# Kernel optimization log

Measured on AMD Instinct MI355X. Metric: run time of the kernel, lower is better.

The kernel has to match this reference:

```python
import jax, jax.numpy as jnp
import numpy as np

N = 100000
IN_F = 165
HID = 128
E = 1600000


def gcn_conv(x, W, b, src, dst, n):
    # PyG GCNConv: h = x @ W; add self-loops; symmetric norm D^-1/2 A D^-1/2; aggregate; + bias
    h = x @ W  # [n, out]
    src_sl = jnp.concatenate([src, jnp.arange(n)])
    dst_sl = jnp.concatenate([dst, jnp.arange(n)])
    deg = jax.ops.segment_sum(jnp.ones_like(src_sl, dtype=h.dtype), dst_sl, num_segments=n)
    dinv = jnp.where(deg > 0, jax.lax.rsqrt(deg), 0.0)
    norm = dinv[src_sl] * dinv[dst_sl]  # [e+n]
    msg = h[src_sl] * norm[:, None]
    out = jax.ops.segment_sum(msg, dst_sl, num_segments=n)
    return out + b


def setup_inputs() -> dict:
    key = jax.random.key(0)
    k = jax.random.split(key, 8)
    x = jax.random.normal(k[0], (N, IN_F), dtype=jnp.float32)
    edge_index = jax.random.randint(k[1], (2, E), 0, N)
    s1 = 1.0 / np.sqrt(IN_F)
    s2 = 1.0 / np.sqrt(HID)
    W1 = jax.random.uniform(k[2], (IN_F, HID), jnp.float32, -s1, s1)
    b1 = jnp.zeros((HID,), jnp.float32)
    W2 = jax.random.uniform(k[3], (HID, HID), jnp.float32, -s2, s2)
    b2 = jnp.zeros((HID,), jnp.float32)
    Wc = jax.random.uniform(k[4], (HID, 2), jnp.float32, -s2, s2)
    bc = jax.random.uniform(k[5], (2,), jnp.float32, -s2, s2)
    return {"x": x, "edge_index": edge_index, "W1": W1, "b1": b1,
            "W2": W2, "b2": b2, "Wc": Wc, "bc": bc}


def reference(x, edge_index, W1, b1, W2, b2, Wc, bc):
    src, dst = edge_index[0], edge_index[1]
    h = jax.nn.relu(gcn_conv(x, W1, b1, src, dst, N))
    # dropout inactive (eval mode)
    h = jax.nn.relu(gcn_conv(h, W2, b2, src, dst, N))
    return h @ Wc + bc
```

## Files before the change

### kernel.cpp

```cpp
#include <hip/hip_runtime.h>


typedef _Float16 half8 __attribute__((ext_vector_type(8)));
typedef float floatx4 __attribute__((ext_vector_type(4)));
typedef float f4u __attribute__((ext_vector_type(4), aligned(4)));

#define SLOT_C 64
#define BCAP 4608
#define NBKT 391
#define CHUNK 4096

__global__ __launch_bounds__(256) void multisplit_k(const int* __restrict__ src,
                                                    const int* __restrict__ dst, int e,
                                                    int* __restrict__ bcnt,
                                                    int2* __restrict__ edges2) {
  __shared__ int lhist[NBKT];
  __shared__ int lbase[NBKT];
  __shared__ int lcur[NBKT];
  int t = threadIdx.x;
  int e0 = blockIdx.x * CHUNK;
  int e1 = min(e0 + CHUNK, e);
  for (int b = t; b < NBKT; b += 256) { lhist[b] = 0; lcur[b] = 0; }
  __syncthreads();
  for (int i = e0 + t; i < e1; i += 256)
    atomicAdd(&lhist[dst[i] >> 8], 1);
  __syncthreads();
  for (int b = t; b < NBKT; b += 256) {
    int h = lhist[b];
    lbase[b] = h ? atomicAdd(&bcnt[b], h) : 0;
  }
  __syncthreads();
  for (int i = e0 + t; i < e1; i += 256) {
    int d = dst[i];
    int b = d >> 8;
    int p = lbase[b] + atomicAdd(&lcur[b], 1);
    if (p < BCAP) edges2[(size_t)b * BCAP + p] = make_int2(src[i], d);
  }
}

__global__ __launch_bounds__(256) void csr_from_bins_k(const int2* __restrict__ edges2,
                                                       const int* __restrict__ bcnt,
                                                       int* __restrict__ cnt_g,
                                                       int* __restrict__ csr,
                                                       float* __restrict__ dinv, int n) {
  __shared__ int lcnt[256];
  int b = blockIdx.x;
  int node0 = b << 8;
  int t = threadIdx.x;
  lcnt[t] = 0;
  __syncthreads();
  int ec = min(bcnt[b], BCAP);
  const int2* ebase = edges2 + (size_t)b * BCAP;
  for (int i = t; i < ec; i += 256) {
    int2 ed = ebase[i];
    int p = atomicAdd(&lcnt[ed.y - node0], 1);
    if (p < SLOT_C) csr[((size_t)ed.y << 6) + p] = ed.x;
  }
  __syncthreads();
  int node = node0 + t;
  if (node < n) {
    int c = lcnt[t];
    cnt_g[node] = c;
    dinv[node] = rsqrtf((float)(c + 1));
  }
}

__global__ void w_split_k(const float* __restrict__ W, int K, int Kpad,
                          _Float16* __restrict__ WhT, _Float16* __restrict__ WlT) {
  int idx = blockIdx.x * blockDim.x + threadIdx.x;
  if (idx >= 128 * Kpad) return;
  int c = idx / Kpad, k = idx - c * Kpad;
  float v = (k < K) ? W[(size_t)k * 128 + c] : 0.f;
  _Float16 h = (_Float16)v;
  WhT[idx] = h;
  WlT[idx] = (_Float16)(v - (float)h);
}

template <bool AHALF>
__global__ __launch_bounds__(256) void gemm_f16_k(const void* __restrict__ Av,
                                                  const _Float16* __restrict__ WhT,
                                                  const _Float16* __restrict__ WlT,
                                                  const float* __restrict__ rowscale,
                                                  _Float16* __restrict__ out,
                                                  int n, int K, int Kpad) {
  int wave = threadIdx.x >> 6, lane = threadIdx.x & 63;
  int m = lane & 15, quad = lane >> 4;
  int rowblk = blockIdx.x >> 1;
  int cbase = (blockIdx.x & 1) * 4;
  int rowbase = rowblk * 64 + wave * 16;
  int ra = min(rowbase + m, n - 1);

  floatx4 acc[4];
#pragma unroll
  for (int c = 0; c < 4; ++c) acc[c] = (floatx4){0.f, 0.f, 0.f, 0.f};

  const int nslab = Kpad >> 5;

  f4u xa0, xa1, xb0, xb1;
  half8 ha, hb;

  auto loadA = [&](int s, f4u& x0, f4u& x1, half8& h) {
    int k0 = (s << 5) + quad * 8;
    if constexpr (AHALF) {
      const _Float16* arow = (const _Float16*)Av + (size_t)ra * K;
      h = *(const half8*)(arow + k0);
    } else {
      const float* arow = (const float*)Av + (size_t)ra * K;
      if ((s << 5) + 32 <= K) {
        x0 = *(const f4u*)(arow + k0);
        x1 = *(const f4u*)(arow + k0 + 4);
      } else {
#pragma unroll
        for (int j = 0; j < 4; ++j) { int kk = k0 + j;     kk = kk < K ? kk : K - 1; x0[j] = arow[kk]; }
#pragma unroll
        for (int j = 0; j < 4; ++j) { int kk = k0 + 4 + j; kk = kk < K ? kk : K - 1; x1[j] = arow[kk]; }
      }
    }
  };

  auto loadW = [&](int s, half8 (&wh)[4], half8 (&wl)[4]) {
    int k0 = (s << 5) + quad * 8;
#pragma unroll
    for (int c = 0; c < 4; ++c) {
      size_t o = (size_t)((cbase + c) * 16 + m) * Kpad + k0;
      wh[c] = *(const half8*)(WhT + o);
      wl[c] = *(const half8*)(WlT + o);
    }
  };

  auto doSlab = [&](const half8 (&wh)[4], const half8 (&wl)[4],
                    const f4u& x0, const f4u& x1, const half8& h) {
    half8 ah, al;
    if constexpr (AHALF) {
      ah = h;
    } else {
#pragma unroll
      for (int j = 0; j < 8; ++j) {
        float v = (j < 4) ? x0[j] : x1[j - 4];
        _Float16 hh = (_Float16)v;
        ah[j] = hh;
        al[j] = (_Float16)(v - (float)hh);
      }
    }
#pragma unroll
    for (int c = 0; c < 4; ++c) {
      acc[c] = __builtin_amdgcn_mfma_f32_16x16x32_f16(ah, wh[c], acc[c], 0, 0, 0);
      acc[c] = __builtin_amdgcn_mfma_f32_16x16x32_f16(ah, wl[c], acc[c], 0, 0, 0);
      if constexpr (!AHALF)
        acc[c] = __builtin_amdgcn_mfma_f32_16x16x32_f16(al, wh[c], acc[c], 0, 0, 0);
    }
  };

  loadA(0, xa0, xa1, ha);
  for (int s = 0; s < nslab; s += 2) {
    half8 wh0[4], wl0[4];
    loadW(s, wh0, wl0);
    loadA(s + 1, xb0, xb1, hb);
    doSlab(wh0, wl0, xa0, xa1, ha);
    half8 wh1[4], wl1[4];
    loadW(s + 1, wh1, wl1);
    if (s + 2 < nslab) loadA(s + 2, xa0, xa1, ha);
    doSlab(wh1, wl1, xb0, xb1, hb);
  }

#pragma unroll
  for (int i = 0; i < 4; ++i) {
    int row = rowbase + quad * 4 + i;
    if (row < n) {
      float di = rowscale ? rowscale[row] : 1.0f;
#pragma unroll
      for (int c = 0; c < 4; ++c)
        out[(size_t)row * 128 + (cbase + c) * 16 + m] = (_Float16)(acc[c][i] * di);
    }
  }
}

template <bool CLS>
__global__ __launch_bounds__(256) void aggregate_k(const _Float16* __restrict__ g,
                                                   const int* __restrict__ cnt,
                                                   const int* __restrict__ csr,
                                                   const float* __restrict__ dinv,
                                                   const float* __restrict__ bias,
                                                   const float* __restrict__ Wc,
                                                   const float* __restrict__ bc,
                                                   _Float16* __restrict__ out16,
                                                   float* __restrict__ out32, int n) {
  int wave = threadIdx.x >> 6;
  int lane = threadIdx.x & 63;
  int i = blockIdx.x * 4 + wave;
  if (i >= n) return;
  int qtr = lane >> 4;
  int l16 = lane & 15;
  int f = l16 * 8;

  float acc[8];
#pragma unroll
  for (int j = 0; j < 8; ++j) acc[j] = 0.f;

  int deg = min(cnt[i], SLOT_C);
  size_t s0 = (size_t)i << 6;

  if (deg > 0) {
    int last = deg - 1;
    for (int eb = 0; eb < deg; eb += 16) {
#pragma unroll
      for (int k = 0; k < 4; ++k) {
        int ee = eb + 4 * k + qtr;
        float w = (ee <= last) ? 1.f : 0.f;
        int ec = (ee <= last) ? ee : last;
        int srow = csr[s0 + ec];
        half8 v = *(const half8*)&g[(size_t)srow * 128 + f];
#pragma unroll
        for (int j = 0; j < 8; ++j) acc[j] = fmaf(w, (float)v[j], acc[j]);
      }
    }
#pragma unroll
    for (int j = 0; j < 8; ++j) {
      acc[j] += __shfl_xor(acc[j], 16, 64);
      acc[j] += __shfl_xor(acc[j], 32, 64);
    }
  }

  half8 self = *(const half8*)&g[(size_t)i * 128 + f];
  float di = dinv[i];
  float4 b0 = *(const float4*)&bias[f];
  float4 b1 = *(const float4*)&bias[f + 4];
  float bv[8] = {b0.x, b0.y, b0.z, b0.w, b1.x, b1.y, b1.z, b1.w};
  float r[8];
#pragma unroll
  for (int j = 0; j < 8; ++j)
    r[j] = fmaxf((acc[j] + (float)self[j]) * di + bv[j], 0.f);

  if (!CLS) {
    if (qtr == 0) {
      half8 o;
#pragma unroll
      for (int j = 0; j < 8; ++j) o[j] = (_Float16)(r[j] * di);
      *(half8*)&out16[(size_t)i * 128 + f] = o;
    }
  } else {
    float c0v = 0.f, c1v = 0.f;
#pragma unroll
    for (int q = 0; q < 4; ++q) {
      float4 wv = *(const float4*)&Wc[f * 2 + q * 4];
      c0v += r[q * 2] * wv.x + r[q * 2 + 1] * wv.z;
      c1v += r[q * 2] * wv.y + r[q * 2 + 1] * wv.w;
    }
#pragma unroll
    for (int off = 8; off > 0; off >>= 1) {
      c0v += __shfl_down(c0v, off, 16);
      c1v += __shfl_down(c1v, off, 16);
    }
    if (lane == 0) {
      out32[(size_t)i * 2 + 0] = c0v + bc[0];
      out32[(size_t)i * 2 + 1] = c1v + bc[1];
    }
  }
}

extern "C" void kernel_launch(void* const* d_in, const int* in_sizes, int n_in,
                              void* d_out, int out_size, void* d_ws, size_t ws_size,
                              hipStream_t stream) {
  const float* x  = (const float*)d_in[0];
  const int*   ei = (const int*)d_in[1];
  const float* W1 = (const float*)d_in[2];
  const float* b1 = (const float*)d_in[3];
  const float* W2 = (const float*)d_in[4];
  const float* b2 = (const float*)d_in[5];
  const float* Wc = (const float*)d_in[6];
  const float* bc = (const float*)d_in[7];
  float* out = (float*)d_out;

  const int IN_F = 165;
  const int KP1 = 192;
  const int n = in_sizes[0] / IN_F;
  const int e = in_sizes[1] / 2;
  const int* src = ei;
  const int* dst = ei + e;

  char* ws = (char*)d_ws;
  size_t off = 0;
  auto alloc = [&](size_t bytes) -> void* {
    void* p = ws + off;
    off += (bytes + 255) & ~(size_t)255;
    return p;
  };
  _Float16* bufA = (_Float16*)alloc((size_t)n * 128 * 2);
  _Float16* bufB = (_Float16*)alloc((size_t)n * 128 * 2);
  int*   csr  = (int*)alloc((size_t)n * SLOT_C * 4);
  int2*  edges2 = (int2*)alloc((size_t)NBKT * BCAP * 8);
  int*   cnt  = (int*)alloc((size_t)n * 4);
  int*   bcnt = (int*)alloc((size_t)NBKT * 4);
  float* dinv = (float*)alloc((size_t)n * 4);
  _Float16* w1h = (_Float16*)alloc((size_t)128 * KP1 * 2);
  _Float16* w1l = (_Float16*)alloc((size_t)128 * KP1 * 2);
  _Float16* w2h = (_Float16*)alloc((size_t)128 * 128 * 2);
  _Float16* w2l = (_Float16*)alloc((size_t)128 * 128 * 2);

  hipMemsetAsync(bcnt, 0, (size_t)NBKT * 4, stream);

  const int tb = 256;
  w_split_k<<<(128 * KP1 + tb - 1) / tb, tb, 0, stream>>>(W1, IN_F, KP1, w1h, w1l);
  w_split_k<<<(128 * 128 + tb - 1) / tb, tb, 0, stream>>>(W2, 128, 128, w2h, w2l);

  multisplit_k<<<(e + CHUNK - 1) / CHUNK, 256, 0, stream>>>(src, dst, e, bcnt, edges2);
  csr_from_bins_k<<<NBKT, 256, 0, stream>>>(edges2, bcnt, cnt, csr, dinv, n);

  const int gemmgrid = 2 * ((n + 63) / 64);
  gemm_f16_k<false><<<gemmgrid, 256, 0, stream>>>(x, w1h, w1l, dinv, bufA, n, IN_F, KP1);
  aggregate_k<false><<<(n + 3) / 4, 256, 0, stream>>>(bufA, cnt, csr, dinv, b1, nullptr, nullptr,
                                                      bufB, nullptr, n);
  gemm_f16_k<true><<<gemmgrid, 256, 0, stream>>>(bufB, w2h, w2l, nullptr, bufA, n, 128, 128);
  aggregate_k<true><<<(n + 3) / 4, 256, 0, stream>>>(bufA, cnt, csr, dinv, b2, Wc, bc,
                                                     nullptr, out, n);
}
```

Measured before the change: 415.3 us.

## Compute all 128 output columns per GEMM block to reuse A loads

```diff
diff --git a/kernel.cpp b/kernel.cpp
--- a/kernel.cpp
+++ b/kernel.cpp
@@ -77,22 +77,20 @@
 }
 
 template <bool AHALF>
-__global__ __launch_bounds__(256) void gemm_f16_k(const void* __restrict__ Av,
-                                                  const _Float16* __restrict__ WhT,
-                                                  const _Float16* __restrict__ WlT,
-                                                  const float* __restrict__ rowscale,
-                                                  _Float16* __restrict__ out,
-                                                  int n, int K, int Kpad) {
+__global__ __launch_bounds__(256, 4) void gemm_f16_k(const void* __restrict__ Av,
+                                                     const _Float16* __restrict__ WhT,
+                                                     const _Float16* __restrict__ WlT,
+                                                     const float* __restrict__ rowscale,
+                                                     _Float16* __restrict__ out,
+                                                     int n, int K, int Kpad) {
   int wave = threadIdx.x >> 6, lane = threadIdx.x & 63;
   int m = lane & 15, quad = lane >> 4;
-  int rowblk = blockIdx.x >> 1;
-  int cbase = (blockIdx.x & 1) * 4;
-  int rowbase = rowblk * 64 + wave * 16;
+  int rowbase = blockIdx.x * 64 + wave * 16;
   int ra = min(rowbase + m, n - 1);
 
-  floatx4 acc[4];
-#pragma unroll
-  for (int c = 0; c < 4; ++c) acc[c] = (floatx4){0.f, 0.f, 0.f, 0.f};
+  floatx4 acc[8];
+#pragma unroll
+  for (int c = 0; c < 8; ++c) acc[c] = (floatx4){0.f, 0.f, 0.f, 0.f};
 
   const int nslab = Kpad >> 5;
 
@@ -118,49 +116,55 @@
     }
   };
 
-  auto loadW = [&](int s, half8 (&wh)[4], half8 (&wl)[4]) {
-    int k0 = (s << 5) + quad * 8;
-#pragma unroll
-    for (int c = 0; c < 4; ++c) {
-      size_t o = (size_t)((cbase + c) * 16 + m) * Kpad + k0;
-      wh[c] = *(const half8*)(WhT + o);
-      wl[c] = *(const half8*)(WlT + o);
-    }
-  };
-
-  auto doSlab = [&](const half8 (&wh)[4], const half8 (&wl)[4],
-                    const f4u& x0, const f4u& x1, const half8& h) {
+  auto doSlab = [&](int s, bool pf, const f4u& cx0, const f4u& cx1, const half8& ch,
+                    f4u& px0, f4u& px1, half8& ph) {
     half8 ah, al;
     if constexpr (AHALF) {
-      ah = h;
+      ah = ch;
     } else {
 #pragma unroll
       for (int j = 0; j < 8; ++j) {
-        float v = (j < 4) ? x0[j] : x1[j - 4];
+        float v = (j < 4) ? cx0[j] : cx1[j - 4];
         _Float16 hh = (_Float16)v;
         ah[j] = hh;
         al[j] = (_Float16)(v - (float)hh);
       }
     }
+    int k0 = (s << 5) + quad * 8;
+    half8 wh0[4], wl0[4], wh1[4], wl1[4];
 #pragma unroll
     for (int c = 0; c < 4; ++c) {
-      acc[c] = __builtin_amdgcn_mfma_f32_16x16x32_f16(ah, wh[c], acc[c], 0, 0, 0);
-      acc[c] = __builtin_amdgcn_mfma_f32_16x16x32_f16(ah, wl[c], acc[c], 0, 0, 0);
+      size_t o = (size_t)(c * 16 + m) * Kpad + k0;
+      wh0[c] = *(const half8*)(WhT + o);
+      wl0[c] = *(const half8*)(WlT + o);
+    }
+#pragma unroll
+    for (int c = 0; c < 4; ++c) {
+      size_t o = (size_t)((4 + c) * 16 + m) * Kpad + k0;
+      wh1[c] = *(const half8*)(WhT + o);
+      wl1[c] = *(const half8*)(WlT + o);
+    }
+    if (pf) loadA(s + 1, px0, px1, ph);
+#pragma unroll
+    for (int c = 0; c < 4; ++c) {
+      acc[c] = __builtin_amdgcn_mfma_f32_16x16x32_f16(ah, wh0[c], acc[c], 0, 0, 0);
+      acc[c] = __builtin_amdgcn_mfma_f32_16x16x32_f16(ah, wl0[c], acc[c], 0, 0, 0);
       if constexpr (!AHALF)
-        acc[c] = __builtin_amdgcn_mfma_f32_16x16x32_f16(al, wh[c], acc[c], 0, 0, 0);
+        acc[c] = __builtin_amdgcn_mfma_f32_16x16x32_f16(al, wh0[c], acc[c], 0, 0, 0);
+    }
+#pragma unroll
+    for (int c = 0; c < 4; ++c) {
+      acc[4 + c] = __builtin_amdgcn_mfma_f32_16x16x32_f16(ah, wh1[c], acc[4 + c], 0, 0, 0);
+      acc[4 + c] = __builtin_amdgcn_mfma_f32_16x16x32_f16(ah, wl1[c], acc[4 + c], 0, 0, 0);
+      if constexpr (!AHALF)
+        acc[4 + c] = __builtin_amdgcn_mfma_f32_16x16x32_f16(al, wh1[c], acc[4 + c], 0, 0, 0);
     }
   };
 
   loadA(0, xa0, xa1, ha);
   for (int s = 0; s < nslab; s += 2) {
-    half8 wh0[4], wl0[4];
-    loadW(s, wh0, wl0);
-    loadA(s + 1, xb0, xb1, hb);
-    doSlab(wh0, wl0, xa0, xa1, ha);
-    half8 wh1[4], wl1[4];
-    loadW(s + 1, wh1, wl1);
-    if (s + 2 < nslab) loadA(s + 2, xa0, xa1, ha);
-    doSlab(wh1, wl1, xb0, xb1, hb);
+    doSlab(s, true, xa0, xa1, ha, xb0, xb1, hb);
+    doSlab(s + 1, s + 2 < nslab, xb0, xb1, hb, xa0, xa1, ha);
   }
 
 #pragma unroll
@@ -169,8 +173,8 @@
     if (row < n) {
       float di = rowscale ? rowscale[row] : 1.0f;
 #pragma unroll
-      for (int c = 0; c < 4; ++c)
-        out[(size_t)row * 128 + (cbase + c) * 16 + m] = (_Float16)(acc[c][i] * di);
+      for (int c = 0; c < 8; ++c)
+        out[(size_t)row * 128 + c * 16 + m] = (_Float16)(acc[c][i] * di);
     }
   }
 }
@@ -306,7 +310,7 @@
   multisplit_k<<<(e + CHUNK - 1) / CHUNK, 256, 0, stream>>>(src, dst, e, bcnt, edges2);
   csr_from_bins_k<<<NBKT, 256, 0, stream>>>(edges2, bcnt, cnt, csr, dinv, n);
 
-  const int gemmgrid = 2 * ((n + 63) / 64);
+  const int gemmgrid = (n + 63) / 64;
   gemm_f16_k<false><<<gemmgrid, 256, 0, stream>>>(x, w1h, w1l, dinv, bufA, n, IN_F, KP1);
   aggregate_k<false><<<(n + 3) / 4, 256, 0, stream>>>(bufA, cnt, csr, dinv, b1, nullptr, nullptr,
                                                       bufB, nullptr, n);
```

New measurement: 457.0 us. 10.0% more time.
